# Kernel tuning notes

Measured on AMD Instinct MI355X. Metric: run time of the kernel, lower is better.

The kernel has to match this reference:

```python
import jax, jax.numpy as jnp
import numpy as np

N_NODES = 100000
N_EDGES = 400000
N_GRAPHS = 4000
IN_DIM = 128
HID = 512
N_DESC = 200
N_CLASSES = 2


def setup_inputs() -> dict:
    key = jax.random.key(0)
    ks = jax.random.split(key, 16)
    features = jax.random.normal(ks[0], (N_NODES, IN_DIM), jnp.float32)
    descriptors = jax.random.normal(ks[1], (N_GRAPHS, N_DESC), jnp.float32)
    src = jax.random.randint(ks[2], (N_EDGES,), 0, N_NODES)
    dst = jax.random.randint(ks[3], (N_EDGES,), 0, N_NODES)
    node2graph = jnp.sort(jax.random.randint(ks[4], (N_NODES,), 0, N_GRAPHS))

    def unif(k, shape, fan_out):
        stdv = 1.0 / np.sqrt(fan_out)
        return jax.random.uniform(k, shape, jnp.float32, -stdv, stdv)

    # GCN layer params (torch init: uniform(-1/sqrt(out), 1/sqrt(out)))
    W1 = unif(ks[5], (IN_DIM, HID), HID)
    b1 = unif(ks[6], (HID,), HID)
    W2 = unif(ks[7], (HID, HID), HID)
    b2 = unif(ks[8], (HID,), HID)
    # MLP head (torch Linear default init: uniform(-1/sqrt(fan_in), ...))
    lw1 = unif(ks[9], (HID + N_DESC, 500), HID + N_DESC)
    lb1 = unif(ks[10], (500,), HID + N_DESC)
    lw2 = unif(ks[11], (500, 100), 500)
    lb2 = unif(ks[12], (100,), 500)
    cw = unif(ks[13], (100, N_CLASSES), 100)
    cb = unif(ks[14], (N_CLASSES,), 100)
    return {"features": features, "descriptors": descriptors, "src": src,
            "dst": dst, "node2graph": node2graph, "W1": W1, "b1": b1,
            "W2": W2, "b2": b2, "lw1": lw1, "lb1": lb1, "lw2": lw2,
            "lb2": lb2, "cw": cw, "cb": cb}


def reference(features, descriptors, src, dst, node2graph,
              W1, b1, W2, b2, lw1, lb1, lw2, lb2, cw, cb):
    N = features.shape[0]
    B = descriptors.shape[0]

    def gcn(h, W, b):
        hW = h @ W                                    # [N, F_out]
        # copy_src + sum: gather source features per edge, scatter-sum to dst
        agg = jax.ops.segment_sum(hW[src], dst, num_segments=N)
        return jax.nn.relu(agg + b)

    h = gcn(features, W1, b1)                         # dropout skipped (eval)
    h = gcn(h, W2, b2)

    # dgl.mean_nodes: per-graph mean over nodes
    sums = jax.ops.segment_sum(h, node2graph, num_segments=B)     # [B, HID]
    counts = jax.ops.segment_sum(jnp.ones((N,), h.dtype), node2graph,
                                 num_segments=B)
    hg = sums / jnp.maximum(counts, 1.0)[:, None]

    x = jnp.concatenate([hg, descriptors], axis=1)    # [B, HID+N_DESC]
    x = jax.nn.relu(x @ lw1 + lb1)
    x = jax.nn.relu(x @ lw2 + lb2)
    return x @ cw + cb                                # [B, n_classes]
```

## Files before the change

kernel.cpp:

```cpp
#include <hip/hip_runtime.h>
#include <hip/hip_bf16.h>

#define N_NODES  100000
#define N_EDGES  400000
#define N_GRAPHS 4000
#define IN_DIM   128
#define HID      512
#define N_DESC   200
#define N_CLASSES 2
#define MLP1_OUT 500
#define MLP2_OUT 100
#define XIN_DIM  (HID + N_DESC)
#define XIN_PAD  768

#define SCAN_CHUNK 1024
#define NCHK ((N_NODES + SCAN_CHUNK - 1) / SCAN_CHUNK)

typedef __hip_bfloat16  bf16;
typedef __hip_bfloat162 bf16x2;
typedef short s8v  __attribute__((ext_vector_type(8)));
typedef float f32x4 __attribute__((ext_vector_type(4)));

__device__ __forceinline__ float ldf(const float* p, size_t i) { return p[i]; }
__device__ __forceinline__ float ldf(const bf16* p, size_t i)  { return __bfloat162float(p[i]); }

__device__ __forceinline__ short f2bs(float x) {
    bf16 h = __float2bfloat16(x);
    return __builtin_bit_cast(short, h);
}

__device__ __forceinline__ void gld16(const short* g, short* l) {
    __builtin_amdgcn_global_load_lds(
        (const __attribute__((address_space(1))) unsigned int*)g,
        (__attribute__((address_space(3))) unsigned int*)l, 16, 0, 0);
}

__global__ __launch_bounds__(256)
void detect_dtype_kernel(const unsigned* __restrict__ words, unsigned nw,
                         int* __restrict__ flag)
{
    __shared__ int s_cnt;
    if (threadIdx.x == 0) s_cnt = 0;
    __syncthreads();
    const int SAMPLES = 2048;
    int sane = 0;
    for (int i = threadIdx.x; i < SAMPLES; i += 256) {
        size_t idx = (size_t)(((unsigned long long)i * 2654435761ull) % nw);
        unsigned w = words[idx];
        float f = __uint_as_float((w & 0xFFFFu) << 16);
        float a = fabsf(f);
        if (f == 0.0f || (a > 1e-8f && a < 1e8f)) sane++;
    }
    atomicAdd(&s_cnt, sane);
    __syncthreads();
    if (threadIdx.x == 0) *flag = (s_cnt * 10 > SAMPLES * 6) ? 1 : 0;
}

template<typename FT>
__device__ __forceinline__
void prep_body(int i, const FT* W1, const FT* W2, const FT* lw1, const FT* lw2,
               const FT* b1, const FT* b2, const FT* lb1, const FT* lb2,
               short* W1t, short* W2t, short* lw1t, short* lw2t,
               float* b1f, float* b2f, float* lb1f, float* lb2f)
{
    if (i < 65536) {
        int n = i >> 7, k = i & 127;
        W1t[i] = f2bs(ldf(W1, (size_t)k * HID + n));
        return;
    }
    i -= 65536;
    if (i < 262144) {
        int n = i >> 9, k = i & 511;
        W2t[i] = f2bs(ldf(W2, (size_t)k * HID + n));
        return;
    }
    i -= 262144;
    if (i < 393216) {
        int n = i / XIN_PAD, k = i - n * XIN_PAD;
        lw1t[i] = (n < MLP1_OUT && k < XIN_DIM)
                      ? f2bs(ldf(lw1, (size_t)k * MLP1_OUT + n)) : (short)0;
        return;
    }
    i -= 393216;
    if (i < 65536) {
        int n = i >> 9, k = i & 511;
        lw2t[i] = (n < MLP2_OUT && k < MLP1_OUT)
                      ? f2bs(ldf(lw2, (size_t)k * MLP2_OUT + n)) : (short)0;
        return;
    }
    i -= 65536;
    if (i < 512) { b1f[i] = ldf(b1, i); return; }
    i -= 512;
    if (i < 512) { b2f[i] = ldf(b2, i); return; }
    i -= 512;
    if (i < 512) { lb1f[i] = (i < MLP1_OUT) ? ldf(lb1, i) : 0.f; return; }
    i -= 512;
    if (i < 128) { lb2f[i] = (i < MLP2_OUT) ? ldf(lb2, i) : 0.f; return; }
}

__global__ __launch_bounds__(256)
void prep_weights_kernel(const void* __restrict__ W1, const void* __restrict__ W2,
                         const void* __restrict__ lw1, const void* __restrict__ lw2,
                         const void* __restrict__ b1, const void* __restrict__ b2,
                         const void* __restrict__ lb1, const void* __restrict__ lb2,
                         short* __restrict__ W1t, short* __restrict__ W2t,
                         short* __restrict__ lw1t, short* __restrict__ lw2t,
                         float* __restrict__ b1f, float* __restrict__ b2f,
                         float* __restrict__ lb1f, float* __restrict__ lb2f,
                         const int* __restrict__ flag)
{
    int i = blockIdx.x * 256 + threadIdx.x;
    if (*flag == 0)
        prep_body<float>(i, (const float*)W1, (const float*)W2, (const float*)lw1,
                         (const float*)lw2, (const float*)b1, (const float*)b2,
                         (const float*)lb1, (const float*)lb2,
                         W1t, W2t, lw1t, lw2t, b1f, b2f, lb1f, lb2f);
    else
        prep_body<bf16>(i, (const bf16*)W1, (const bf16*)W2, (const bf16*)lw1,
                        (const bf16*)lw2, (const bf16*)b1, (const bf16*)b2,
                        (const bf16*)lb1, (const bf16*)lb2,
                        W1t, W2t, lw1t, lw2t, b1f, b2f, lb1f, lb2f);
}

__global__ __launch_bounds__(256)
void deg_kernel(const int* __restrict__ dst, int* __restrict__ deg)
{
    int e = blockIdx.x * 256 + threadIdx.x;
    if (e < N_EDGES) atomicAdd(&deg[dst[e]], 1);
}

__global__ __launch_bounds__(256)
void scan_partial_kernel(const int* __restrict__ deg, int* __restrict__ part)
{
    int c = blockIdx.x, t = threadIdx.x;
    int i0 = c * SCAN_CHUNK + t * 4;
    int s = 0;
#pragma unroll
    for (int j = 0; j < 4; j++) {
        int i = i0 + j;
        if (i < N_NODES) s += deg[i];
    }
    __shared__ int red[256];
    red[t] = s;
    __syncthreads();
    for (int off = 128; off > 0; off >>= 1) {
        if (t < off) red[t] += red[t + off];
        __syncthreads();
    }
    if (t == 0) part[c] = red[0];
}

__global__ void scan_parts_kernel(int* __restrict__ part, int* __restrict__ edge_start)
{
    int run = 0;
    for (int c = 0; c < NCHK; c++) { int v = part[c]; part[c] = run; run += v; }
    edge_start[N_NODES] = run;
}

__global__ __launch_bounds__(256)
void scan_final_kernel(const int* __restrict__ deg, const int* __restrict__ part,
                       int* __restrict__ edge_start, int* __restrict__ cursor)
{
    int c = blockIdx.x, t = threadIdx.x;
    int i0 = c * SCAN_CHUNK + t * 4;
    int d[4];
    int tsum = 0;
#pragma unroll
    for (int j = 0; j < 4; j++) {
        int i = i0 + j;
        d[j] = (i < N_NODES) ? deg[i] : 0;
        tsum += d[j];
    }
    __shared__ int s[256];
    s[t] = tsum;
    __syncthreads();
    for (int off = 1; off < 256; off <<= 1) {
        int v = (t >= off) ? s[t - off] : 0;
        __syncthreads();
        s[t] += v;
        __syncthreads();
    }
    int run = part[c] + s[t] - tsum;
#pragma unroll
    for (int j = 0; j < 4; j++) {
        int i = i0 + j;
        if (i < N_NODES) { edge_start[i] = run; cursor[i] = run; run += d[j]; }
    }
}

__global__ __launch_bounds__(256)
void fill_kernel(const int* __restrict__ src, const int* __restrict__ dst,
                 int* __restrict__ cursor, int* __restrict__ csr_src)
{
    int e = blockIdx.x * 256 + threadIdx.x;
    if (e >= N_EDGES) return;
    int p = atomicAdd(&cursor[dst[e]], 1);
    csr_src[p] = src[e];
}

__global__ __launch_bounds__(256)
void gstart_kernel(const int* __restrict__ n2g, int* __restrict__ gstart)
{
    int n = blockIdx.x * 256 + threadIdx.x;
    if (n > N_NODES) return;
    if (n == N_NODES) {
        int last = n2g[N_NODES - 1];
        for (int g = last + 1; g <= N_GRAPHS; g++) gstart[g] = N_NODES;
        return;
    }
    int v = n2g[n];
    int prev = (n == 0) ? -1 : n2g[n - 1];
    for (int g = prev + 1; g <= v; g++) gstart[g] = n;
}

__global__ __launch_bounds__(256)
void gather_feat_kernel(const void* __restrict__ feat_, const int* __restrict__ edge_start,
                        const int* __restrict__ csr_src, bf16* __restrict__ agg1,
                        const int* __restrict__ flag)
{
    int n = blockIdx.x * 4 + (threadIdx.x >> 6);
    if (n >= N_NODES) return;
    int lane = threadIdx.x & 63;
    int e0 = edge_start[n], e1 = edge_start[n + 1];
    float2 acc = {0.f, 0.f};
    if (*flag == 0) {
        const float* feat = (const float*)feat_;
        for (int i = e0; i < e1; i++) {
            int s = csr_src[i];
            float2 f = ((const float2*)(feat + (size_t)s * IN_DIM))[lane];
            acc.x += f.x; acc.y += f.y;
        }
    } else {
        const bf16* feat = (const bf16*)feat_;
        for (int i = e0; i < e1; i++) {
            int s = csr_src[i];
            float2 f = __bfloat1622float2(((const bf16x2*)(feat + (size_t)s * IN_DIM))[lane]);
            acc.x += f.x; acc.y += f.y;
        }
    }
    bf16x2 p;
    p.x = __float2bfloat16(acc.x);
    p.y = __float2bfloat16(acc.y);
    ((bf16x2*)(agg1 + (size_t)n * IN_DIM))[lane] = p;
}

__global__ __launch_bounds__(256)
void gather_h_kernel(const bf16* __restrict__ h1, const int* __restrict__ edge_start,
                     const int* __restrict__ csr_src, bf16* __restrict__ aggc)
{
    int n = blockIdx.x * 4 + (threadIdx.x >> 6);
    if (n >= N_NODES) return;
    int lane = threadIdx.x & 63;
    int e0 = edge_start[n], e1 = edge_start[n + 1];
    float acc[8];
#pragma unroll
    for (int j = 0; j < 8; j++) acc[j] = 0.f;
    for (int i = e0; i < e1; i++) {
        int s = csr_src[i];
        float4 r = ((const float4*)(h1 + (size_t)s * HID))[lane];
        const bf16x2* p = (const bf16x2*)&r;
#pragma unroll
        for (int q = 0; q < 4; q++) {
            float2 f = __bfloat1622float2(p[q]);
            acc[2 * q] += f.x; acc[2 * q + 1] += f.y;
        }
    }
    s8v s;
#pragma unroll
    for (int j = 0; j < 8; j++) s[j] = f2bs(acc[j]);
    ((float4*)(aggc + (size_t)n * HID))[lane] = __builtin_bit_cast(float4, s);
}

template<int NCT>
__global__ __launch_bounds__(256)
void mfma_gemm_kernel(const short* __restrict__ A, const short* __restrict__ Bt,
                      const float* __restrict__ biasf, bf16* __restrict__ Cout,
                      int M, int K, int nrt)
{
    __shared__ short smem[17408];
    short* As = smem;
    short* Bs = smem + 8192;
    short* Cs = smem;

    const int b  = blockIdx.x;
    const int r8 = b & 7;
    const int t  = b >> 3;
    const int x  = (t / NCT) * 8 + r8;
    const int y  = t % NCT;
    if (x >= nrt) return;
    const int row0 = x * 128;
    const int col0 = y * 128;

    const int tid  = threadIdx.x;
    const int lane = tid & 63;
    const int w    = tid >> 6;
    const int wr = w >> 1, wc = w & 1;
    const int m  = lane & 15, q = lane >> 4;

    const int dr = lane >> 3;
    const int dc = ((lane & 7) ^ dr) * 8;
    const short* ga[4];
    const short* gb[4];
    short* la[4];
    short* lb[4];
#pragma unroll
    for (int c = 0; c < 4; c++) {
        int r = (w * 4 + c) * 8 + dr;
        ga[c] = A  + (size_t)(row0 + r) * K + dc;
        gb[c] = Bt + (size_t)(col0 + r) * K + dc;
        la[c] = As + (w * 4 + c) * 512;
        lb[c] = Bs + (w * 4 + c) * 512;
    }

    const int sa = ((q ^ (m & 7)) * 8);

    f32x4 acc[4][4];
#pragma unroll
    for (int i = 0; i < 4; i++)
#pragma unroll
        for (int j = 0; j < 4; j++) acc[i][j] = {0.f, 0.f, 0.f, 0.f};

    for (int k0 = 0; k0 < K; k0 += 64) {
#pragma unroll
        for (int c = 0; c < 4; c++) gld16(ga[c], la[c]);
#pragma unroll
        for (int c = 0; c < 4; c++) gld16(gb[c], lb[c]);
#pragma unroll
        for (int c = 0; c < 4; c++) { ga[c] += 64; gb[c] += 64; }
        __syncthreads();

#pragma unroll
        for (int kq = 0; kq < 2; kq++) {
            const int so = sa ^ (kq * 32);
            s8v av[4], bv[4];
#pragma unroll
            for (int rt = 0; rt < 4; rt++)
                av[rt] = *(const s8v*)&As[(wr * 64 + rt * 16 + m) * 64 + so];
#pragma unroll
            for (int ct = 0; ct < 4; ct++)
                bv[ct] = *(const s8v*)&Bs[(wc * 64 + ct * 16 + m) * 64 + so];
#pragma unroll
            for (int rt = 0; rt < 4; rt++)
#pragma unroll
                for (int ct = 0; ct < 4; ct++)
                    acc[rt][ct] = __builtin_amdgcn_mfma_f32_16x16x32_bf16(
                        av[rt], bv[ct], acc[rt][ct], 0, 0, 0);
        }
        __syncthreads();
    }

#pragma unroll
    for (int rt = 0; rt < 4; rt++) {
#pragma unroll
        for (int ct = 0; ct < 4; ct++) {
            int lcol = wc * 64 + ct * 16 + m;
            float bv = biasf[col0 + lcol];
#pragma unroll
            for (int reg = 0; reg < 4; reg++) {
                int lrow = wr * 64 + rt * 16 + q * 4 + reg;
                float v = acc[rt][ct][reg] + bv;
                v = v > 0.f ? v : 0.f;
                Cs[lrow * 136 + lcol] = f2bs(v);
            }
        }
    }
    __syncthreads();

#pragma unroll
    for (int it = 0; it < 8; it++) {
        int idx = it * 256 + tid;
        int r = idx >> 4;
        int c = (idx & 15) * 8;
        int row = row0 + r;
        if (row < M)
            *(float4*)&Cout[(size_t)row * HID + col0 + c] =
                *(const float4*)&Cs[r * 136 + c];
    }
}

__global__ __launch_bounds__(256)
void pool_graph_kernel(const bf16* __restrict__ h2, const int* __restrict__ gstart,
                       float* __restrict__ hg)
{
    int g = blockIdx.x * 4 + (threadIdx.x >> 6);
    if (g >= N_GRAPHS) return;
    int lane = threadIdx.x & 63;
    int s0 = gstart[g], s1 = gstart[g + 1];
    float acc[8];
#pragma unroll
    for (int j = 0; j < 8; j++) acc[j] = 0.f;
    for (int n = s0; n < s1; n++) {
        float4 r = ((const float4*)(h2 + (size_t)n * HID))[lane];
        const bf16x2* p = (const bf16x2*)&r;
#pragma unroll
        for (int q = 0; q < 4; q++) {
            float2 f = __bfloat1622float2(p[q]);
            acc[2 * q] += f.x; acc[2 * q + 1] += f.y;
        }
    }
    float* orow = hg + (size_t)g * HID + lane * 8;
    ((float4*)orow)[0] = make_float4(acc[0], acc[1], acc[2], acc[3]);
    ((float4*)orow)[1] = make_float4(acc[4], acc[5], acc[6], acc[7]);
}

__global__ __launch_bounds__(256)
void build_xin_kernel(const float* __restrict__ hg, const int* __restrict__ gstart,
                      const void* __restrict__ desc_, bf16* __restrict__ xinb,
                      const int* __restrict__ flag)
{
    int idx = blockIdx.x * 256 + threadIdx.x;
    if (idx >= N_GRAPHS * XIN_PAD) return;
    int g = idx / XIN_PAD;
    int c = idx - g * XIN_PAD;
    float v;
    if (c < HID) {
        float cnt = (float)(gstart[g + 1] - gstart[g]);
        v = hg[(size_t)g * HID + c] / (cnt > 1.0f ? cnt : 1.0f);
    } else if (c < XIN_DIM) {
        size_t di = (size_t)g * N_DESC + (c - HID);
        v = (*flag == 0) ? ((const float*)desc_)[di]
                         : __bfloat162float(((const bf16*)desc_)[di]);
    } else {
        v = 0.f;
    }
    xinb[idx] = __float2bfloat16(v);
}

__global__ __launch_bounds__(256)
void final_layer_kernel(const bf16* __restrict__ x2b, const void* __restrict__ cw_,
                        const void* __restrict__ cb_, void* __restrict__ out_,
                        const int* __restrict__ flag)
{
    int i = blockIdx.x * 256 + threadIdx.x;
    if (i >= N_GRAPHS * N_CLASSES) return;
    int r = i >> 1, c = i & 1;
    const bf16* x = x2b + (size_t)r * HID;
    if (*flag == 0) {
        const float* cw = (const float*)cw_;
        float acc = ((const float*)cb_)[c];
#pragma unroll 4
        for (int k = 0; k < MLP2_OUT; k++)
            acc += __bfloat162float(x[k]) * cw[k * N_CLASSES + c];
        ((float*)out_)[i] = acc;
    } else {
        const bf16* cw = (const bf16*)cw_;
        float acc = __bfloat162float(((const bf16*)cb_)[c]);
#pragma unroll 4
        for (int k = 0; k < MLP2_OUT; k++)
            acc += __bfloat162float(x[k]) * __bfloat162float(cw[k * N_CLASSES + c]);
        ((bf16*)out_)[i] = __float2bfloat16(acc);
    }
}

static inline size_t align_up(size_t x, size_t a) { return (x + a - 1) & ~(a - 1); }
static inline int swgrid(int nrt, int nct) { return ((nrt + 7) / 8) * 8 * nct; }

extern "C" void kernel_launch(void* const* d_in, const int* in_sizes, int n_in,
                              void* d_out, int out_size, void* d_ws, size_t ws_size,
                              hipStream_t stream)
{
    const void* features    = d_in[0];
    const void* descriptors = d_in[1];
    const int*  src         = (const int*)d_in[2];
    const int*  dst         = (const int*)d_in[3];
    const int*  node2graph  = (const int*)d_in[4];
    const void* W1          = d_in[5];
    const void* b1          = d_in[6];
    const void* W2          = d_in[7];
    const void* b2          = d_in[8];
    const void* lw1         = d_in[9];
    const void* lb1         = d_in[10];
    const void* lw2         = d_in[11];
    const void* lb2         = d_in[12];
    const void* cw          = d_in[13];
    const void* cb          = d_in[14];
    (void)in_sizes; (void)n_in; (void)out_size; (void)ws_size;

    char* ws = (char*)d_ws;
    size_t off = 0;
    bf16* agg1 = (bf16*)(ws + off);
    bf16* aggc = (bf16*)(ws + off);
    bf16* xinb = (bf16*)(ws + off);
    bf16* x1b  = (bf16*)(ws + off + (size_t)8 * 1024 * 1024);
    bf16* x2b  = (bf16*)(ws + off + (size_t)16 * 1024 * 1024);
    off = align_up(off + (size_t)N_NODES * HID * sizeof(bf16), 256);
    bf16* h1 = (bf16*)(ws + off);
    bf16* h2 = (bf16*)(ws + off);
    off = align_up(off + (size_t)N_NODES * HID * sizeof(bf16), 256);
    float* hg = (float*)(ws + off);
    off = align_up(off + (size_t)N_GRAPHS * HID * sizeof(float), 256);
    int* dflag = (int*)(ws + off);          off = align_up(off + 256, 256);
    int* edge_start = (int*)(ws + off);     off = align_up(off + (N_NODES + 1) * 4, 256);
    int* cursor = (int*)(ws + off);         off = align_up(off + N_NODES * 4, 256);
    int* csr_src = (int*)(ws + off);        off = align_up(off + N_EDGES * 4, 256);
    int* part = (int*)(ws + off);           off = align_up(off + NCHK * 4, 256);
    int* deg = (int*)(ws + off);            off = align_up(off + N_NODES * 4, 256);
    int* gstart = (int*)(ws + off);         off = align_up(off + (N_GRAPHS + 1) * 4, 256);
    short* W1t  = (short*)(ws + off);       off = align_up(off + (size_t)HID * IN_DIM * 2, 256);
    short* W2t  = (short*)(ws + off);       off = align_up(off + (size_t)HID * HID * 2, 256);
    short* lw1t = (short*)(ws + off);       off = align_up(off + (size_t)512 * XIN_PAD * 2, 256);
    short* lw2t = (short*)(ws + off);       off = align_up(off + (size_t)128 * HID * 2, 256);
    float* b1f  = (float*)(ws + off);       off = align_up(off + 512 * 4, 256);
    float* b2f  = (float*)(ws + off);       off = align_up(off + 512 * 4, 256);
    float* lb1f = (float*)(ws + off);       off = align_up(off + 512 * 4, 256);
    float* lb2f = (float*)(ws + off);       off = align_up(off + 128 * 4, 256);

    detect_dtype_kernel<<<1, 256, 0, stream>>>(
        (const unsigned*)features, (unsigned)(N_NODES * IN_DIM / 2), dflag);

    {
        int nblk = (788096 + 255) / 256;
        prep_weights_kernel<<<nblk, 256, 0, stream>>>(
            W1, W2, lw1, lw2, b1, b2, lb1, lb2,
            W1t, W2t, lw1t, lw2t, b1f, b2f, lb1f, lb2f, dflag);
    }

    hipMemsetAsync(deg, 0, N_NODES * 4, stream);
    deg_kernel<<<(N_EDGES + 255) / 256, 256, 0, stream>>>(dst, deg);
    scan_partial_kernel<<<NCHK, 256, 0, stream>>>(deg, part);
    scan_parts_kernel<<<1, 1, 0, stream>>>(part, edge_start);
    scan_final_kernel<<<NCHK, 256, 0, stream>>>(deg, part, edge_start, cursor);
    fill_kernel<<<(N_EDGES + 255) / 256, 256, 0, stream>>>(src, dst, cursor, csr_src);
    gstart_kernel<<<(N_NODES + 256) / 256, 256, 0, stream>>>(node2graph, gstart);

    gather_feat_kernel<<<N_NODES / 4, 256, 0, stream>>>(
        features, edge_start, csr_src, agg1, dflag);
    {
        int nrt = (N_NODES + 127) / 128;
        mfma_gemm_kernel<4><<<swgrid(nrt, 4), 256, 0, stream>>>(
            (const short*)agg1, W1t, b1f, h1, N_NODES, IN_DIM, nrt);
    }

    gather_h_kernel<<<N_NODES / 4, 256, 0, stream>>>(h1, edge_start, csr_src, aggc);
    {
        int nrt = (N_NODES + 127) / 128;
        mfma_gemm_kernel<4><<<swgrid(nrt, 4), 256, 0, stream>>>(
            (const short*)aggc, W2t, b2f, h2, N_NODES, HID, nrt);
    }
    pool_graph_kernel<<<N_GRAPHS / 4, 256, 0, stream>>>(h2, gstart, hg);

    {
        int nthr = (N_GRAPHS * XIN_PAD + 255) / 256;
        build_xin_kernel<<<nthr, 256, 0, stream>>>(
            hg, gstart, descriptors, xinb, dflag);
    }
    {
        int nrt = (N_GRAPHS + 127) / 128;
        mfma_gemm_kernel<4><<<swgrid(nrt, 4), 256, 0, stream>>>(
            (const short*)xinb, lw1t, lb1f, x1b, N_GRAPHS, XIN_PAD, nrt);
    }
    {
        int nrt = (N_GRAPHS + 127) / 128;
        mfma_gemm_kernel<1><<<swgrid(nrt, 1), 256, 0, stream>>>(
            (const short*)x1b, lw2t, lb2f, x2b, N_GRAPHS, HID, nrt);
    }
    {
        int nthr = (N_GRAPHS * N_CLASSES + 255) / 256;
        final_layer_kernel<<<nthr, 256, 0, stream>>>(
            x2b, cw, cb, d_out, dflag);
    }
}
```

Before: 467.6 us.

## Double-buffer GEMM LDS tiles with K-step 32 and prefetch overlap

Restructures the MFMA GEMM main loop to use two LDS buffers with a K-tile of 32 instead of a single 64-wide buffer. The next tile's global-to-LDS loads are issued before computing on the current one, and manual vmcnt waits plus raw barriers replace the full syncthreads. The goal is to hide global load latency behind MFMA work. In exchange there are twice as many loop iterations and barriers, and the swizzle pattern changes for the narrower rows.

```diff
diff --git a/kernel.cpp b/kernel.cpp
--- a/kernel.cpp
+++ b/kernel.cpp
@@ -34,6 +34,8 @@
         (const __attribute__((address_space(1))) unsigned int*)g,
         (__attribute__((address_space(3))) unsigned int*)l, 16, 0, 0);
 }
+
+#define MEMFENCE asm volatile("" ::: "memory")
 
 __global__ __launch_bounds__(256)
 void detect_dtype_kernel(const unsigned* __restrict__ words, unsigned nw,
@@ -278,15 +280,13 @@
                       int M, int K, int nrt)
 {
     __shared__ short smem[17408];
-    short* As = smem;
-    short* Bs = smem + 8192;
     short* Cs = smem;
 
     const int b  = blockIdx.x;
     const int r8 = b & 7;
-    const int t  = b >> 3;
-    const int x  = (t / NCT) * 8 + r8;
-    const int y  = t % NCT;
+    const int t0 = b >> 3;
+    const int x  = (t0 / NCT) * 8 + r8;
+    const int y  = t0 % NCT;
     if (x >= nrt) return;
     const int row0 = x * 128;
     const int col0 = y * 128;
@@ -297,22 +297,22 @@
     const int wr = w >> 1, wc = w & 1;
     const int m  = lane & 15, q = lane >> 4;
 
-    const int dr = lane >> 3;
-    const int dc = ((lane & 7) ^ dr) * 8;
-    const short* ga[4];
-    const short* gb[4];
-    short* la[4];
-    short* lb[4];
-#pragma unroll
-    for (int c = 0; c < 4; c++) {
-        int r = (w * 4 + c) * 8 + dr;
+    const int rr = lane >> 2;
+    const int dc = ((lane & 3) ^ ((lane >> 3) & 3)) * 8;
+    const short* ga[2];
+    const short* gb[2];
+    short* la[2];
+    short* lb[2];
+#pragma unroll
+    for (int c = 0; c < 2; c++) {
+        int r = (w * 2 + c) * 16 + rr;
         ga[c] = A  + (size_t)(row0 + r) * K + dc;
         gb[c] = Bt + (size_t)(col0 + r) * K + dc;
-        la[c] = As + (w * 4 + c) * 512;
-        lb[c] = Bs + (w * 4 + c) * 512;
-    }
-
-    const int sa = ((q ^ (m & 7)) * 8);
+        la[c] = smem + (w * 2 + c) * 512;
+        lb[c] = smem + 4096 + (w * 2 + c) * 512;
+    }
+
+    const int so = (q ^ ((m >> 1) & 3)) * 8;
 
     f32x4 acc[4][4];
 #pragma unroll
@@ -320,33 +320,50 @@
 #pragma unroll
         for (int j = 0; j < 4; j++) acc[i][j] = {0.f, 0.f, 0.f, 0.f};
 
-    for (int k0 = 0; k0 < K; k0 += 64) {
-#pragma unroll
-        for (int c = 0; c < 4; c++) gld16(ga[c], la[c]);
-#pragma unroll
-        for (int c = 0; c < 4; c++) gld16(gb[c], lb[c]);
-#pragma unroll
-        for (int c = 0; c < 4; c++) { ga[c] += 64; gb[c] += 64; }
-        __syncthreads();
-
-#pragma unroll
-        for (int kq = 0; kq < 2; kq++) {
-            const int so = sa ^ (kq * 32);
-            s8v av[4], bv[4];
-#pragma unroll
-            for (int rt = 0; rt < 4; rt++)
-                av[rt] = *(const s8v*)&As[(wr * 64 + rt * 16 + m) * 64 + so];
+#pragma unroll
+    for (int c = 0; c < 2; c++) {
+        gld16(ga[c], la[c]);
+        gld16(gb[c], lb[c]);
+        ga[c] += 32; gb[c] += 32;
+    }
+
+    const int NT = K >> 5;
+    for (int t = 0; t < NT; ++t) {
+        const int boff = (t & 1) * 8192;
+        if (t + 1 < NT) {
+            const int noff = 8192 - boff;
+#pragma unroll
+            for (int c = 0; c < 2; c++) {
+                gld16(ga[c], la[c] + noff);
+                gld16(gb[c], lb[c] + noff);
+                ga[c] += 32; gb[c] += 32;
+            }
+            asm volatile("s_waitcnt vmcnt(4)" ::: "memory");
+        } else {
+            asm volatile("s_waitcnt vmcnt(0)" ::: "memory");
+        }
+        __builtin_amdgcn_s_barrier();
+        MEMFENCE;
+
+        const short* Ab = smem + boff;
+        const short* Bb = smem + boff + 4096;
+        s8v av[4], bv[4];
+#pragma unroll
+        for (int rt = 0; rt < 4; rt++)
+            av[rt] = *(const s8v*)&Ab[(wr * 64 + rt * 16 + m) * 32 + so];
+#pragma unroll
+        for (int ct = 0; ct < 4; ct++)
+            bv[ct] = *(const s8v*)&Bb[(wc * 64 + ct * 16 + m) * 32 + so];
+#pragma unroll
+        for (int rt = 0; rt < 4; rt++)
 #pragma unroll
             for (int ct = 0; ct < 4; ct++)
-                bv[ct] = *(const s8v*)&Bs[(wc * 64 + ct * 16 + m) * 64 + so];
-#pragma unroll
-            for (int rt = 0; rt < 4; rt++)
-#pragma unroll
-                for (int ct = 0; ct < 4; ct++)
-                    acc[rt][ct] = __builtin_amdgcn_mfma_f32_16x16x32_bf16(
-                        av[rt], bv[ct], acc[rt][ct], 0, 0, 0);
-        }
-        __syncthreads();
+                acc[rt][ct] = __builtin_amdgcn_mfma_f32_16x16x32_bf16(
+                    av[rt], bv[ct], acc[rt][ct], 0, 0, 0);
+
+        MEMFENCE;
+        __builtin_amdgcn_s_barrier();
+        MEMFENCE;
     }
 
 #pragma unroll
```

Result: faster. 455.9 us (-2.5%).
